# Optimization experiments

Measured on AMD Instinct MI355X. Metric: run time of the kernel, lower is better.

## Reference

```python
import jax, jax.numpy as jnp
import numpy as np

NUM_HEADS = 3
WIN = 7            # window_size (square)
PAD = WIN // 2     # conv / v padding


def setup_inputs() -> dict:
    key = jax.random.key(0)
    ks = jax.random.split(key, 8)
    B, C, H, W = 8, 96, 56, 56
    hd = C // NUM_HEADS  # 32
    x = jax.random.normal(ks[0], (B, C, H, W), jnp.float32)
    # qkv 1x1 conv: weight (3C, C), bias (3C,)
    w_qkv = jax.random.normal(ks[1], (3 * C, C), jnp.float32) * (C ** -0.5)
    b_qkv = jax.random.normal(ks[2], (3 * C,), jnp.float32) * 0.01
    fan_in = 2 * hd * WIN * WIN
    w_dm = jax.random.normal(ks[3], (WIN * WIN, 2 * hd, WIN, WIN), jnp.float32) * (fan_in ** -0.5)
    b_dm = jax.random.normal(ks[4], (WIN * WIN,), jnp.float32) * 0.01
    bias_table = jax.random.normal(ks[5], (WIN * WIN, NUM_HEADS), jnp.float32) * 0.02
    # proj 1x1 conv
    w_proj = jax.random.normal(ks[6], (C, C), jnp.float32) * (C ** -0.5)
    b_proj = jax.random.normal(ks[7], (C,), jnp.float32) * 0.01
    return dict(x=x, w_qkv=w_qkv, b_qkv=b_qkv, w_dm=w_dm, b_dm=b_dm,
                bias_table=bias_table, w_proj=w_proj, b_proj=b_proj)


def reference(x, w_qkv, b_qkv, w_dm, b_dm, bias_table, w_proj, b_proj):
    B, C, H, W = x.shape
    nh = NUM_HEADS
    hd = C // nh
    scale = hd ** -0.5

    # qkv 1x1 conv -> (B, 3, nh, hd, H, W)
    qkv = jnp.einsum('oc,bchw->bohw', w_qkv, x) + b_qkv[None, :, None, None]
    qkv = qkv.reshape(B, 3, nh, hd, H, W)
    q, k, v = qkv[:, 0], qkv[:, 1], qkv[:, 2]

    qk = jnp.concatenate([(q * scale).reshape(B * nh, hd, H, W),
                          k.reshape(B * nh, hd, H, W)], axis=1)
    attn = jax.lax.conv_general_dilated(
        qk, w_dm, window_strides=(1, 1), padding=[(PAD, PAD), (PAD, PAD)],
        dimension_numbers=('NCHW', 'OIHW', 'NCHW')) + b_dm[None, :, None, None]
    attn = attn.reshape(B, nh, WIN * WIN, H, W)

    # relative position bias, broadcast over spatial dims
    attn = attn + bias_table.T.reshape(1, nh, WIN * WIN, 1, 1)
    attn = jax.nn.softmax(attn, axis=2)

    # gather sliding windows of v from a zero-padded tensor
    v_pad = jnp.pad(v, ((0, 0), (0, 0), (0, 0), (PAD, PAD), (PAD, PAD)))
    vw = jnp.stack([v_pad[..., i // WIN:i // WIN + H, i % WIN:i % WIN + W]
                    for i in range(WIN * WIN)], axis=3)

    # weighted sum over window dim, merge heads back to channels
    out = jnp.sum(vw * attn[:, :, None], axis=3).reshape(B, C, H, W)

    # output 1x1 projection (dropout p=0 -> identity)
    out = jnp.einsum('oc,bchw->bohw', w_proj, out) + b_proj[None, :, None, None]
    return out
```

## Files before the change

kernel.cpp:

```cpp
#include <hip/hip_runtime.h>
#include <hip/hip_bf16.h>
#include <stdint.h>

#define BATCH 8
#define CCH 96
#define NH 3
#define HD 32
#define HGT 56
#define WID 56
#define HW 3136
#define WIN 7
#define KK 49
#define PADR 3
#define NIMG 24
#define C2 64

typedef const float* fp32p;
typedef __attribute__((ext_vector_type(8))) short bf16x8;
typedef __attribute__((ext_vector_type(16))) float f32x16;
typedef unsigned short ushort_t;

__device__ __forceinline__ float bf2f_bits(unsigned u){ return __uint_as_float(u << 16); }
__device__ __forceinline__ ushort_t f2bf_bits(float f){
  __hip_bfloat16 hb = __float2bfloat16(f);
  return *(ushort_t*)&hb;
}

__global__ void prep_kernel(fp32p w_dm, fp32p b_dm, fp32p bias_table,
                            fp32p w_qkv, fp32p w_proj,
                            __hip_bfloat16* __restrict__ w3, float* __restrict__ bias3,
                            ushort_t* __restrict__ wq3, ushort_t* __restrict__ wp3){
  int t = blockIdx.x * 256 + threadIdx.x;
  if (t < 200704){
    int j   = t & 7;
    int l   = (t >> 3) & 63;
    int mt  = (t >> 9) & 1;
    int cb  = (t >> 10) & 1;
    int pt  = t >> 11;
    int pass = pt / KK, tap = pt % KK;
    int o  = mt*32 + (l & 31);
    int ch = pass*32 + cb*16 + (l >> 5)*8 + j;
    float v = 0.f;
    if (o < KK) v = w_dm[((size_t)(o*C2 + ch))*KK + tap];
    w3[t] = __float2bfloat16(v);
  } else if (t < 200896){
    int t2 = t - 200704;
    int h = t2 >> 6;
    int o = t2 & 63;
    bias3[t2] = (o < KK) ? (b_dm[o] + bias_table[o*NH + h]) : -1e30f;
  } else if (t < 200896 + 27648){
    int i = t - 200896;
    int j = i & 7, l = (i >> 3) & 63;
    int rest = i >> 9;
    int mt = rest % 9, k = rest / 9;
    int o = mt*32 + (l & 31);
    int c = k*16 + (l >> 5)*8 + j;
    wq3[i] = f2bf_bits(w_qkv[o*CCH + c]);
  } else if (t < 200896 + 27648 + 9216){
    int i = t - 200896 - 27648;
    int j = i & 7, l = (i >> 3) & 63;
    int rest = i >> 9;
    int mt = rest % 3, k = rest / 3;
    int o = mt*32 + (l & 31);
    int c = k*16 + (l >> 5)*8 + j;
    wp3[i] = f2bf_bits(w_proj[o*CCH + c]);
  }
}

__global__ __launch_bounds__(256) void xt_kernel(fp32p x, ushort_t* __restrict__ xbf){
  __shared__ float lds[128*97];
  int px0 = blockIdx.x * 128;
  int tid = threadIdx.x;
  #pragma unroll
  for (int it = 0; it < 48; ++it){
    int s = tid + it*256;
    int px = s & 127;
    int c  = s >> 7;
    int gpx = px0 + px;
    int b = gpx / HW, pp = gpx % HW;
    lds[px*97 + c] = x[((size_t)b*CCH + c)*HW + pp];
  }
  __syncthreads();
  #pragma unroll
  for (int it = 0; it < 6; ++it){
    int s = tid + it*256;
    int j  = s % 12;
    int px = s / 12;
    unsigned u[4];
    #pragma unroll
    for (int q = 0; q < 4; ++q){
      float f0 = lds[px*97 + j*8 + 2*q];
      float f1 = lds[px*97 + j*8 + 2*q + 1];
      u[q] = (unsigned)f2bf_bits(f0) | ((unsigned)f2bf_bits(f1) << 16);
    }
    uint4 w4; w4.x=u[0]; w4.y=u[1]; w4.z=u[2]; w4.w=u[3];
    *(uint4*)((char*)xbf + ((size_t)(px0+px)*96 + j*8)*2) = w4;
  }
}

__global__ __launch_bounds__(64) void qkv_kernel(const ushort_t* __restrict__ xbf,
    const ushort_t* __restrict__ wq3, fp32p b_qkv,
    ushort_t* __restrict__ qplane, ushort_t* __restrict__ kplane,
    ushort_t* __restrict__ v2){
  int wid = blockIdx.x;
  int g  = wid / 784;
  int pt = wid % 784;
  int l = threadIdx.x & 63, col = l & 31, hi = l >> 5;
  int px = pt*32 + col;
  int b = px / HW, pp = px % HW;

  bf16x8 B[6];
  const char* bb = (const char*)xbf + (size_t)px*192 + hi*16;
  #pragma unroll
  for (int k = 0; k < 6; ++k) B[k] = *(const bf16x8*)(bb + k*32);

  f32x16 acc[3];
  #pragma unroll
  for (int m = 0; m < 3; ++m)
    #pragma unroll
    for (int r = 0; r < 16; ++r) acc[m][r] = 0.f;

  #pragma unroll
  for (int k = 0; k < 6; ++k){
    #pragma unroll
    for (int m = 0; m < 3; ++m){
      bf16x8 A = *(const bf16x8*)((const char*)wq3 + ((size_t)((k*9 + g*3 + m)*64 + l))*16);
      acc[m] = __builtin_amdgcn_mfma_f32_32x32x16_bf16(A, B[k], acc[m], 0, 0, 0);
    }
  }
  const float scale = 0.17677669529663687f;
  ushort_t* plane = (g == 0) ? qplane : (g == 1 ? kplane : v2);
  #pragma unroll
  for (int m = 0; m < 3; ++m){
    ushort_t* dst = plane + ((size_t)((b*NH + m)*HW + pp))*32;
    #pragma unroll
    for (int q = 0; q < 4; ++q){
      int base = 8*q + 4*hi;
      float v0 = acc[m][q*4+0] + b_qkv[g*96 + m*32 + base + 0];
      float v1 = acc[m][q*4+1] + b_qkv[g*96 + m*32 + base + 1];
      float v2f = acc[m][q*4+2] + b_qkv[g*96 + m*32 + base + 2];
      float v3 = acc[m][q*4+3] + b_qkv[g*96 + m*32 + base + 3];
      if (g == 0){ v0 *= scale; v1 *= scale; v2f *= scale; v3 *= scale; }
      uint2 pk;
      pk.x = (unsigned)f2bf_bits(v0) | ((unsigned)f2bf_bits(v1) << 16);
      pk.y = (unsigned)f2bf_bits(v2f) | ((unsigned)f2bf_bits(v3) << 16);
      *(uint2*)(&dst[base]) = pk;
    }
  }
}

#define MFMA4K(Ab, Bb) \
  { _Pragma("unroll") for (int nt = 0; nt < 2; ++nt){ \
      acc[0][nt] = __builtin_amdgcn_mfma_f32_32x32x16_bf16(Ab[0], Bb[nt], acc[0][nt], 0, 0, 0); \
      acc[1][nt] = __builtin_amdgcn_mfma_f32_32x32x16_bf16(Ab[1], Bb[nt], acc[1][nt], 0, 0, 0); \
    } }

#define LOADAK(tt, Ab) \
  { const char* An_ = Abase + (size_t)(tt)*4096; \
    Ab[0] = *(const bf16x8*)(An_); \
    Ab[1] = *(const bf16x8*)(An_ + 1024); }

#define LOADBK(tt, Bb) \
  { int ky_ = (tt) / 7, kx_ = (tt) - ky_*7; \
    _Pragma("unroll") for (int nt = 0; nt < 2; ++nt){ \
      int xp_ = nt*32 + col + kx_; if (xp_ > 61) xp_ = 61; \
      int base_ = ((row + ky_)*64 + xp_)*64; \
      int sx_ = (xp_ & 3) ^ ((xp_ >> 2) & 3); \
      Bb[nt] = *(const bf16x8*)(&smem[base_ + ((((cbw << 1) | hi) ^ sx_) << 4)]); } }

#define XWRITE(A0v, A1v) \
  { _Pragma("unroll") for (int q = 0; q < 4; ++q){ \
      float4 v4; \
      v4.x=A0v[4*q+0]; v4.y=A0v[4*q+1]; v4.z=A0v[4*q+2]; v4.w=A0v[4*q+3]; \
      *(float4*)((char*)xch + slot_o*256 + (((2*q+hi) ^ xsw)<<4)) = v4; \
      v4.x=A1v[4*q+0]; v4.y=A1v[4*q+1]; v4.z=A1v[4*q+2]; v4.w=A1v[4*q+3]; \
      *(float4*)((char*)xch + slot_o*256 + (((8+2*q+hi) ^ xsw)<<4)) = v4; } }

#define XREAD(A0v, A1v) \
  { _Pragma("unroll") for (int q = 0; q < 4; ++q){ \
      float4 v4 = *(const float4*)((char*)xch + slot_s*256 + (((2*q+hi) ^ xsw)<<4)); \
      A0v[4*q+0]+=v4.x; A0v[4*q+1]+=v4.y; A0v[4*q+2]+=v4.z; A0v[4*q+3]+=v4.w; \
      v4 = *(const float4*)((char*)xch + slot_s*256 + (((8+2*q+hi) ^ xsw)<<4)); \
      A1v[4*q+0]+=v4.x; A1v[4*q+1]+=v4.y; A1v[4*q+2]+=v4.z; A1v[4*q+3]+=v4.w; } }

__global__ __launch_bounds__(256, 3) void attn_kernel(
    const ushort_t* __restrict__ qplane, const ushort_t* __restrict__ kplane,
    const __hip_bfloat16* __restrict__ w3, const float* __restrict__ bias3,
    const ushort_t* __restrict__ v2, ushort_t* __restrict__ tmp2){
  __shared__ char smem[50176];

  int bid = blockIdx.x;
  int n  = bid / 28;
  int y0 = (bid % 28) * 2;
  int b = n / NH, head = n % NH;
  int tid = threadIdx.x;
  int l = tid & 63, w = tid >> 6, hi = l >> 5, col = l & 31;
  int row = w >> 1;
  int cbw = w & 1;

  f32x16 acc[2][2];
  #pragma unroll
  for (int r = 0; r < 16; ++r){
    int rowv = (r & 3) + 8*(r >> 2) + 4*hi;
    float b0 = (cbw == 0) ? bias3[head*64 + rowv] : 0.f;
    float b1 = (cbw == 0) ? bias3[head*64 + 32 + rowv] : 0.f;
    #pragma unroll
    for (int nt = 0; nt < 2; ++nt){ acc[0][nt][r] = b0; acc[1][nt][r] = b1; }
  }

  for (int pass = 0; pass < 2; ++pass){
    if (pass) __syncthreads();
    const char* src = (const char*)(pass ? kplane : qplane) + (size_t)n * HW * 64;
    #pragma unroll
    for (int it = 0; it < 8; ++it){
      int s = tid + it*256;
      int c   = s & 3;
      int xp  = (s >> 2) & 63;
      int rw  = s >> 8;
      int gy = y0 - 3 + rw;
      int gx = xp - 3;
      uint4 val = {0,0,0,0};
      if ((unsigned)gy < HGT && (unsigned)gx < WID)
        val = *(const uint4*)(src + (size_t)(gy*WID + gx)*64 + c*16);
      int sw = (c ^ (xp & 3) ^ ((xp >> 2) & 3)) << 4;
      *(uint4*)(&smem[(rw*64 + xp)*64 + sw]) = val;
    }
    __syncthreads();

    const char* Abase = (const char*)w3 + (size_t)pass*KK*4096 + cbw*2048 + l*16;
    bf16x8 A0[2], A1[2], B0[2], B1[2];
    LOADAK(0, A0); LOADBK(0, B0);
    LOADAK(1, A1); LOADBK(1, B1);
    for (int t = 0; t < 48; t += 2){
      MFMA4K(A0, B0);
      LOADAK(t+2, A0); LOADBK(t+2, B0);
      MFMA4K(A1, B1);
      int t3 = (t+3 < KK) ? (t+3) : 48;
      LOADAK(t3, A1); LOADBK(t3, B1);
    }
    MFMA4K(A0, B0);
  }

  __syncthreads();
  float* xch = (float*)smem;
  int xsw = col & 15;
  {
    int slot_o = row*64 + (1-cbw)*32 + col;
    if (cbw == 0){ XWRITE(acc[0][1], acc[1][1]); }
    else         { XWRITE(acc[0][0], acc[1][0]); }
  }
  __syncthreads();
  f32x16 a0, a1;
  {
    int slot_s = row*64 + cbw*32 + col;
    if (cbw == 0){ XREAD(acc[0][0], acc[1][0]); a0 = acc[0][0]; a1 = acc[1][0]; }
    else         { XREAD(acc[0][1], acc[1][1]); a0 = acc[0][1]; a1 = acc[1][1]; }
  }

  const char* vb = (const char*)v2 + (size_t)n * HW * 64;
  uint4 vreg[8];
  #pragma unroll
  for (int it = 0; it < 8; ++it){
    int s = tid + it*256;
    int xp  = s & 63;
    int c   = (s >> 6) & 3;
    int rw  = s >> 8;
    int gy = y0 - 3 + rw;
    int gx = xp - 3;
    uint4 val = {0,0,0,0};
    if ((unsigned)gy < HGT && (unsigned)gx < WID)
      val = *(const uint4*)(vb + (size_t)(gy*WID + gx)*64 + c*16);
    vreg[it] = val;
  }

  ushort_t* Pp = (ushort_t*)&smem[32768];
  {
    float m = -1e30f;
    #pragma unroll
    for (int r = 0; r < 16; ++r){ m = fmaxf(m, a0[r]); m = fmaxf(m, a1[r]); }
    m = fmaxf(m, __shfl_xor(m, 32));
    float s = 0.f;
    #pragma unroll
    for (int r = 0; r < 16; ++r){
      a0[r] = __expf(a0[r] - m); s += a0[r];
      a1[r] = __expf(a1[r] - m); s += a1[r];
    }
    s += __shfl_xor(s, 32);
    float inv = 1.f / s;
    int pixslot = row*64 + cbw*32 + col;
    ushort_t* Pr = Pp + pixslot*68;
    #pragma unroll
    for (int q = 0; q < 4; ++q){
      int base = 8*q + 4*hi;
      uint2 pk0;
      pk0.x = (unsigned)f2bf_bits(a0[q*4+0]*inv) | ((unsigned)f2bf_bits(a0[q*4+1]*inv) << 16);
      pk0.y = (unsigned)f2bf_bits(a0[q*4+2]*inv) | ((unsigned)f2bf_bits(a0[q*4+3]*inv) << 16);
      *(uint2*)(&Pr[base]) = pk0;
      uint2 pk1;
      pk1.x = (unsigned)f2bf_bits(a1[q*4+0]*inv) | ((unsigned)f2bf_bits(a1[q*4+1]*inv) << 16);
      pk1.y = (unsigned)f2bf_bits(a1[q*4+2]*inv) | ((unsigned)f2bf_bits(a1[q*4+3]*inv) << 16);
      *(uint2*)(&Pr[32 + base]) = pk1;
    }
  }
  __syncthreads();

  #pragma unroll
  for (int it = 0; it < 8; ++it){
    int s = tid + it*256;
    int xp  = s & 63;
    int c   = (s >> 6) & 3;
    int rw  = s >> 8;
    *(uint4*)(&smem[((c*8 + rw)*64 + xp)*16]) = vreg[it];
  }
  __syncthreads();

  int ch2 = tid >> 7;
  int slot = tid & 127;
  int pr = slot >> 6, pxx = slot & 63;
  if (pxx < WID){
    float out[16];
    #pragma unroll
    for (int i = 0; i < 16; ++i) out[i] = 0.f;
    #pragma unroll
    for (int ky = 0; ky < WIN; ++ky){
      #pragma unroll
      for (int kx = 0; kx < WIN; ++kx){
        float pw = bf2f_bits(Pp[slot*68 + ky*7 + kx]);
        int vrow = pr + ky, xp = pxx + kx;
        #pragma unroll
        for (int ci = 0; ci < 2; ++ci){
          int cc = ch2*2 + ci;
          uint4 vv = *(const uint4*)(&smem[((cc*8 + vrow)*64 + xp)*16]);
          unsigned ua[4] = {vv.x, vv.y, vv.z, vv.w};
          #pragma unroll
          for (int q = 0; q < 4; ++q){
            out[ci*8 + 2*q]     = fmaf(pw, __uint_as_float(ua[q] << 16),         out[ci*8 + 2*q]);
            out[ci*8 + 2*q + 1] = fmaf(pw, __uint_as_float(ua[q] & 0xffff0000u), out[ci*8 + 2*q + 1]);
          }
        }
      }
    }
    int pp = (y0 + pr)*WID + pxx;
    ushort_t* dst = tmp2 + ((size_t)(b*HW + pp))*96 + head*32 + ch2*16;
    #pragma unroll
    for (int j2 = 0; j2 < 2; ++j2){
      unsigned u[4];
      #pragma unroll
      for (int q = 0; q < 4; ++q){
        u[q] = (unsigned)f2bf_bits(out[j2*8 + 2*q]) | ((unsigned)f2bf_bits(out[j2*8 + 2*q + 1]) << 16);
      }
      uint4 w4; w4.x=u[0]; w4.y=u[1]; w4.z=u[2]; w4.w=u[3];
      *(uint4*)(&dst[j2*8]) = w4;
    }
  }
}

__global__ __launch_bounds__(64) void proj_kernel(const ushort_t* __restrict__ tmp2,
    const ushort_t* __restrict__ wp3, fp32p b_proj, float* __restrict__ outp){
  int pt = blockIdx.x;
  int l = threadIdx.x & 63, col = l & 31, hi = l >> 5;
  int px = pt*32 + col;
  int b = px / HW, pp = px % HW;

  bf16x8 B[6];
  const char* bb = (const char*)tmp2 + (size_t)px*192 + hi*16;
  #pragma unroll
  for (int k = 0; k < 6; ++k) B[k] = *(const bf16x8*)(bb + k*32);

  f32x16 acc[3];
  #pragma unroll
  for (int m = 0; m < 3; ++m)
    #pragma unroll
    for (int r = 0; r < 16; ++r) acc[m][r] = 0.f;

  #pragma unroll
  for (int k = 0; k < 6; ++k){
    #pragma unroll
    for (int m = 0; m < 3; ++m){
      bf16x8 A = *(const bf16x8*)((const char*)wp3 + ((size_t)((k*3 + m)*64 + l))*16);
      acc[m] = __builtin_amdgcn_mfma_f32_32x32x16_bf16(A, B[k], acc[m], 0, 0, 0);
    }
  }
  #pragma unroll
  for (int m = 0; m < 3; ++m){
    #pragma unroll
    for (int r = 0; r < 16; ++r){
      int o = m*32 + (r & 3) + 8*(r >> 2) + 4*hi;
      outp[((size_t)(b*CCH + o))*HW + pp] = acc[m][r] + b_proj[o];
    }
  }
}

extern "C" void kernel_launch(void* const* d_in, const int* in_sizes, int n_in,
                              void* d_out, int out_size, void* d_ws, size_t ws_size,
                              hipStream_t stream){
  fp32p x          = (fp32p)d_in[0];
  fp32p w_qkv      = (fp32p)d_in[1];
  fp32p b_qkv      = (fp32p)d_in[2];
  fp32p w_dm       = (fp32p)d_in[3];
  fp32p b_dm       = (fp32p)d_in[4];
  fp32p bias_table = (fp32p)d_in[5];
  fp32p w_proj     = (fp32p)d_in[6];
  fp32p b_proj     = (fp32p)d_in[7];

  char* ws = (char*)d_ws;
  const size_t XBF_BYTES   = (size_t)BATCH * HW * 96 * 2;
  const size_t PLANE_BYTES = (size_t)NIMG * HW * 32 * 2;
  const size_t TMP2_BYTES  = (size_t)BATCH * HW * 96 * 2;
  const size_t W3_BYTES    = 200704ull * 2;
  size_t off = 0;
  ushort_t* xbf    = (ushort_t*)(ws + off); off += XBF_BYTES;
  ushort_t* qplane = (ushort_t*)(ws + off); off += PLANE_BYTES;
  ushort_t* kplane = (ushort_t*)(ws + off); off += PLANE_BYTES;
  ushort_t* v2     = (ushort_t*)(ws + off); off += PLANE_BYTES;
  ushort_t* tmp2   = (ushort_t*)(ws + off); off += TMP2_BYTES;
  __hip_bfloat16* w3 = (__hip_bfloat16*)(ws + off); off += W3_BYTES;
  float* bias3     = (float*)(ws + off);    off += 192*4;
  ushort_t* wq3    = (ushort_t*)(ws + off); off += 27648*2;
  ushort_t* wp3    = (ushort_t*)(ws + off); off += 9216*2;

  hipLaunchKernelGGL(prep_kernel, dim3(929), dim3(256), 0, stream,
                     w_dm, b_dm, bias_table, w_qkv, w_proj, w3, bias3, wq3, wp3);
  hipLaunchKernelGGL(xt_kernel, dim3(196), dim3(256), 0, stream, x, xbf);
  hipLaunchKernelGGL(qkv_kernel, dim3(2352), dim3(64), 0, stream,
                     xbf, wq3, b_qkv, qplane, kplane, v2);
  hipLaunchKernelGGL(attn_kernel, dim3(672), dim3(256), 0, stream,
                     qplane, kplane, w3, bias3, v2, tmp2);
  hipLaunchKernelGGL(proj_kernel, dim3(784), dim3(64), 0, stream,
                     tmp2, wp3, b_proj, (float*)d_out);
}
```

Before: 78.04 us.

## Apply softmax probabilities from MFMA registers directly, dropping shared-memory P staging

The normalized attention probabilities stay in the MFMA accumulator registers instead of being packed to bf16 and staged in shared memory. The P·V sum is remapped so each lane handles the window taps it already holds, across all 32 channels. The two half-wave partial sums are then combined with cross-lane shuffles. This removes the 17 KB P buffer, which lets launch bounds rise to 4 blocks per SM, but doubles the per-thread accumulator registers and adds shuffle work.

```diff
diff --git a/kernel.cpp b/kernel.cpp
--- a/kernel.cpp
+++ b/kernel.cpp
@@ -183,11 +183,20 @@
       v4 = *(const float4*)((char*)xch + slot_s*256 + (((8+2*q+hi) ^ xsw)<<4)); \
       A1v[4*q+0]+=v4.x; A1v[4*q+1]+=v4.y; A1v[4*q+2]+=v4.z; A1v[4*q+3]+=v4.w; } }
 
-__global__ __launch_bounds__(256, 3) void attn_kernel(
+#define PVTAP(p_, dl_) \
+  { _Pragma("unroll") for (int cc = 0; cc < 4; ++cc){ \
+      uint4 vv = *(const uint4*)(&smem[cc*8192 + vbase + (dl_)]); \
+      unsigned ua[4] = {vv.x, vv.y, vv.z, vv.w}; \
+      _Pragma("unroll") for (int q = 0; q < 4; ++q){ \
+        out[cc*8 + 2*q]     = fmaf(p_, __uint_as_float(ua[q] << 16),         out[cc*8 + 2*q]); \
+        out[cc*8 + 2*q + 1] = fmaf(p_, __uint_as_float(ua[q] & 0xffff0000u), out[cc*8 + 2*q + 1]); \
+      } } }
+
+__global__ __launch_bounds__(256, 4) void attn_kernel(
     const ushort_t* __restrict__ qplane, const ushort_t* __restrict__ kplane,
     const __hip_bfloat16* __restrict__ w3, const float* __restrict__ bias3,
     const ushort_t* __restrict__ v2, ushort_t* __restrict__ tmp2){
-  __shared__ char smem[50176];
+  __shared__ char smem[32768];
 
   int bid = blockIdx.x;
   int n  = bid / 28;
@@ -273,7 +282,6 @@
     vreg[it] = val;
   }
 
-  ushort_t* Pp = (ushort_t*)&smem[32768];
   {
     float m = -1e30f;
     #pragma unroll
@@ -287,20 +295,10 @@
     }
     s += __shfl_xor(s, 32);
     float inv = 1.f / s;
-    int pixslot = row*64 + cbw*32 + col;
-    ushort_t* Pr = Pp + pixslot*68;
-    #pragma unroll
-    for (int q = 0; q < 4; ++q){
-      int base = 8*q + 4*hi;
-      uint2 pk0;
-      pk0.x = (unsigned)f2bf_bits(a0[q*4+0]*inv) | ((unsigned)f2bf_bits(a0[q*4+1]*inv) << 16);
-      pk0.y = (unsigned)f2bf_bits(a0[q*4+2]*inv) | ((unsigned)f2bf_bits(a0[q*4+3]*inv) << 16);
-      *(uint2*)(&Pr[base]) = pk0;
-      uint2 pk1;
-      pk1.x = (unsigned)f2bf_bits(a1[q*4+0]*inv) | ((unsigned)f2bf_bits(a1[q*4+1]*inv) << 16);
-      pk1.y = (unsigned)f2bf_bits(a1[q*4+2]*inv) | ((unsigned)f2bf_bits(a1[q*4+3]*inv) << 16);
-      *(uint2*)(&Pr[32 + base]) = pk1;
-    }
+    #pragma unroll
+    for (int r = 0; r < 16; ++r) a0[r] *= inv;
+    #pragma unroll
+    for (int r = 0; r < 9; ++r)  a1[r] *= inv;
   }
   __syncthreads();
 
@@ -314,40 +312,48 @@
   }
   __syncthreads();
 
-  int ch2 = tid >> 7;
-  int slot = tid & 127;
-  int pr = slot >> 6, pxx = slot & 63;
+  int pxx = cbw*32 + col;
   if (pxx < WID){
-    float out[16];
-    #pragma unroll
-    for (int i = 0; i < 16; ++i) out[i] = 0.f;
-    #pragma unroll
-    for (int ky = 0; ky < WIN; ++ky){
-      #pragma unroll
-      for (int kx = 0; kx < WIN; ++kx){
-        float pw = bf2f_bits(Pp[slot*68 + ky*7 + kx]);
-        int vrow = pr + ky, xp = pxx + kx;
-        #pragma unroll
-        for (int ci = 0; ci < 2; ++ci){
-          int cc = ch2*2 + ci;
-          uint4 vv = *(const uint4*)(&smem[((cc*8 + vrow)*64 + xp)*16]);
-          unsigned ua[4] = {vv.x, vv.y, vv.z, vv.w};
-          #pragma unroll
-          for (int q = 0; q < 4; ++q){
-            out[ci*8 + 2*q]     = fmaf(pw, __uint_as_float(ua[q] << 16),         out[ci*8 + 2*q]);
-            out[ci*8 + 2*q + 1] = fmaf(pw, __uint_as_float(ua[q] & 0xffff0000u), out[ci*8 + 2*q + 1]);
-          }
-        }
-      }
-    }
-    int pp = (y0 + pr)*WID + pxx;
-    ushort_t* dst = tmp2 + ((size_t)(b*HW + pp))*96 + head*32 + ch2*16;
+    int vbase = (row*64 + pxx)*16;
+    float out[32];
+    #pragma unroll
+    for (int i = 0; i < 32; ++i) out[i] = 0.f;
+
+    #pragma unroll
+    for (int r = 0; r < 16; ++r){
+      const int c0 = (r & 3) + 8*(r >> 2);
+      const int d0 = ((c0)/7)*1024 + ((c0)%7)*16;
+      const int d1 = ((c0+4)/7)*1024 + ((c0+4)%7)*16;
+      int dl = hi ? d1 : d0;
+      float p = a0[r];
+      PVTAP(p, dl);
+    }
+    #pragma unroll
+    for (int r = 0; r < 9; ++r){
+      const int c0 = (r & 3) + 8*(r >> 2);
+      const int o0 = 32 + c0;
+      const int d0 = (o0/7)*1024 + (o0%7)*16;
+      const int d1 = (r == 8) ? d0 : ((o0+4)/7)*1024 + ((o0+4)%7)*16;
+      int dl = hi ? d1 : d0;
+      float p = (r == 8) ? (hi ? 0.f : a1[8]) : a1[r];
+      PVTAP(p, dl);
+    }
+
+    float fin[16];
+    #pragma unroll
+    for (int j = 0; j < 16; ++j){
+      float lo = out[j]      + __shfl_xor(out[j], 32);
+      float hv = out[16 + j] + __shfl_xor(out[16 + j], 32);
+      fin[j] = hi ? hv : lo;
+    }
+    int pp = (y0 + row)*WID + pxx;
+    ushort_t* dst = tmp2 + ((size_t)(b*HW + pp))*96 + head*32 + hi*16;
     #pragma unroll
     for (int j2 = 0; j2 < 2; ++j2){
       unsigned u[4];
       #pragma unroll
       for (int q = 0; q < 4; ++q){
-        u[q] = (unsigned)f2bf_bits(out[j2*8 + 2*q]) | ((unsigned)f2bf_bits(out[j2*8 + 2*q + 1]) << 16);
+        u[q] = (unsigned)f2bf_bits(fin[j2*8 + 2*q]) | ((unsigned)f2bf_bits(fin[j2*8 + 2*q + 1]) << 16);
       }
       uint4 w4; w4.x=u[0]; w4.y=u[1]; w4.z=u[2]; w4.w=u[3];
       *(uint4*)(&dst[j2*8]) = w4;
```

Result: slower. 103.4 us (+32.6%).
